# Kernel tuning notes

Measured on AMD Instinct MI355X. Metric: run time of the kernel, lower is better.

## Reference

```python
import jax, jax.numpy as jnp
import numpy as np

HEADS = 8
D_MODEL = 512

def setup_inputs() -> dict:
    key = jax.random.key(0)
    ks = jax.random.split(key, 7)
    t, w, h, b = 8, 14, 14, 8
    seq = t * w * h + 1  # 1569, includes CLS token
    q = jax.random.normal(ks[0], (seq, b, D_MODEL), jnp.float32)
    k = jax.random.normal(ks[1], (seq, b, D_MODEL), jnp.float32)
    value = jax.random.normal(ks[2], (seq, b, D_MODEL), jnp.float32)
    in_proj_weight = jax.random.normal(ks[3], (3 * D_MODEL, D_MODEL), jnp.float32) * (D_MODEL ** -0.5)
    in_proj_bias = jax.random.normal(ks[4], (3 * D_MODEL,), jnp.float32) * 0.02
    out_w = jax.random.normal(ks[5], (D_MODEL, D_MODEL), jnp.float32) * (D_MODEL ** -0.5)
    out_b = jax.random.normal(ks[6], (D_MODEL,), jnp.float32) * 0.02
    return {"q": q, "k": k, "value": value,
            "in_proj_weight": in_proj_weight, "in_proj_bias": in_proj_bias,
            "out_w": out_w, "out_b": out_b, "t": t, "w": w, "h": h}

def _sdpa(q, k, v):
    # scaled dot-product attention over batched 3D tensors [B, L, dh]
    temp = q.shape[-1] ** 0.5
    scores = jnp.einsum('bqd,bkd->bqk', q, k) / temp
    a = jax.nn.softmax(scores, axis=-1)  # softmax over dim=2 == last dim
    return jnp.einsum('bqk,bkd->bqd', a, v), a

def reference(q, k, value, in_proj_weight, in_proj_bias, out_w, out_b, t, w, h):
    seq, b, c = q.shape
    H, dh, wh = HEADS, c // HEADS, w * h
    q_cls = q[:1]          # [1, b, c] passed through untouched
    x = q[1:]              # [t*wh, b, c]
    qkv = x @ in_proj_weight.T + in_proj_bias  # fused QKV proj
    qq, kk, vv = qkv[..., :c], qkv[..., c:2 * c], qkv[..., 2 * c:]
    to5 = lambda z: z.reshape(t, wh, b, H, dh)
    # spatial stage: batch = (H, b, t), attend over wh
    q_s = to5(qq).transpose(3, 2, 0, 1, 4).reshape(H * b * t, wh, dh)
    k_s = to5(kk).transpose(3, 2, 0, 1, 4).reshape(H * b * t, wh, dh)
    v_s = to5(vv).transpose(3, 2, 0, 1, 4).reshape(H * b * t, wh, dh)
    out_s, attn = _sdpa(q_s, k_s, v_s)
    # temporal stage: batch = (H, b, wh), attend over t; V comes from spatial output
    v_t = out_s.reshape(H, b, t, wh, dh).transpose(0, 1, 3, 2, 4).reshape(H * b * wh, t, dh)
    q_t = to5(qq).transpose(3, 2, 1, 0, 4).reshape(H * b * wh, t, dh)
    k_t = to5(kk).transpose(3, 2, 1, 0, 4).reshape(H * b * wh, t, dh)
    out_t, _ = _sdpa(q_t, k_t, v_t)
    # back to [t*wh, b, c]
    out = out_t.reshape(H, b, wh, t, dh).transpose(3, 2, 1, 0, 4).reshape(t * wh, b, c)
    out = out @ out_w.T + out_b
    return jnp.concatenate([q_cls, out], axis=0), attn
```

## Files before the change

kernel.cpp:

```cpp
#include <hip/hip_runtime.h>
#include <cstdint>
#include <cstddef>

typedef __bf16 bf16;
typedef __bf16 bf16x8 __attribute__((ext_vector_type(8)));
typedef __bf16 bf16x4 __attribute__((ext_vector_type(4)));
typedef float  f32x4  __attribute__((ext_vector_type(4)));

#define MFMA16(a, b, c) __builtin_amdgcn_mfma_f32_16x16x32_bf16(a, b, c, 0, 0, 0)

__device__ __forceinline__ void gl2lds16(const bf16* g, bf16* l) {
  __builtin_amdgcn_global_load_lds(
      (const __attribute__((address_space(1))) void*)g,
      (__attribute__((address_space(3))) void*)l, 16, 0, 0);
}

__device__ __forceinline__ void cvt4(const float* __restrict__ s, bf16* __restrict__ d) {
  f32x4 v = *(const f32x4*)s;
  bf16x4 o;
  o[0] = (bf16)v[0]; o[1] = (bf16)v[1]; o[2] = (bf16)v[2]; o[3] = (bf16)v[3];
  *(bf16x4*)d = o;
}

__global__ __launch_bounds__(256) void prep_kernel(
    const float* __restrict__ q, const float* __restrict__ win,
    const float* __restrict__ wout, float* __restrict__ out0,
    bf16* __restrict__ xb, bf16* __restrict__ wqb, bf16* __restrict__ wob) {
  long u = (long)blockIdx.x * 256 + threadIdx.x;
  const long NX4 = 1605632, NWQ4 = 196608, NWO4 = 65536, NQC4 = 1024;
  if (u < NX4) { cvt4(q + 4096 + u * 4, xb + u * 4); return; }
  u -= NX4;
  if (u < NWQ4) { cvt4(win + u * 4, wqb + u * 4); return; }
  u -= NWQ4;
  if (u < NWO4) { cvt4(wout + u * 4, wob + u * 4); return; }
  u -= NWO4;
  if (u < NQC4) { *(f32x4*)(out0 + u * 4) = *(const f32x4*)(q + u * 4); }
}

template <bool OUTF32>
__global__ __launch_bounds__(256) void gemm_bt(
    const bf16* __restrict__ A, const bf16* __restrict__ Bm,
    const float* __restrict__ bias, bf16* __restrict__ Cb,
    float* __restrict__ Cf, int N, int K, long coff) {
  __shared__ bf16 As[128 * 32];
  __shared__ bf16 Bs[128 * 32];
  const int tid = threadIdx.x;
  const int wid = tid >> 6, lane = tid & 63;
  const int lr = lane & 15, lg = lane >> 4;

  const int nwg = gridDim.x * gridDim.y;
  const int orig = blockIdx.y * gridDim.x + blockIdx.x;
  const int cpx = nwg >> 3;
  const int swz = (orig & 7) * cpx + (orig >> 3);
  const int m0 = (swz / gridDim.x) * 128;
  const int n0 = (swz % gridDim.x) * 128;

  const int wr = wid >> 1, wc = wid & 1;
  const int srow = lane >> 2;
  const int scol = (lane & 3) * 8;

  f32x4 acc[4][4] = {};

  for (int kt = 0; kt < K; kt += 32) {
    __syncthreads();
#pragma unroll
    for (int j = 0; j < 2; ++j) {
      int r0 = wid * 32 + j * 16;
      gl2lds16(A + (size_t)(m0 + r0 + srow) * K + kt + scol, As + r0 * 32);
      gl2lds16(Bm + (size_t)(n0 + r0 + srow) * K + kt + scol, Bs + r0 * 32);
    }
    __syncthreads();

    bf16x8 af[4], bfr[4];
#pragma unroll
    for (int m = 0; m < 4; ++m)
      af[m] = *(const bf16x8*)(As + (wr * 64 + m * 16 + lr) * 32 + lg * 8);
#pragma unroll
    for (int n = 0; n < 4; ++n)
      bfr[n] = *(const bf16x8*)(Bs + (wc * 64 + n * 16 + lr) * 32 + lg * 8);
#pragma unroll
    for (int m = 0; m < 4; ++m)
#pragma unroll
      for (int n = 0; n < 4; ++n)
        acc[m][n] = MFMA16(af[m], bfr[n], acc[m][n]);
  }

#pragma unroll
  for (int m = 0; m < 4; ++m) {
    int row = m0 + wr * 64 + m * 16 + lg * 4;
#pragma unroll
    for (int n = 0; n < 4; ++n) {
      int col = n0 + wc * 64 + n * 16 + lr;
      float bv = bias[col];
#pragma unroll
      for (int i = 0; i < 4; ++i) {
        float v = acc[m][n][i] + bv;
        if (OUTF32) Cf[coff + (size_t)(row + i) * N + col] = v;
        else        Cb[(size_t)(row + i) * N + col] = (bf16)v;
      }
    }
  }
}

__global__ __launch_bounds__(512) void spatial_attn(
    const bf16* __restrict__ qkv, float* __restrict__ attn_out,
    bf16* __restrict__ outs) {
  __shared__ bf16 Kl[224][72];
  __shared__ bf16 Vt[64][232];
  __shared__ bf16 Pl[8][16][232];

  const int tid = threadIdx.x;
  const int wid = tid >> 6, lane = tid & 63;
  const int lr = lane & 15, lg = lane >> 4;
  const int batch = blockIdx.x;
  const int ti = batch & 7;
  const int bb = (batch >> 3) & 7;
  const int h = batch >> 6;

  {
    const int p = (tid >> 3);
    const int c = (tid & 7) * 8;
    bf16 zz = (bf16)0.f;
    for (int r0 = 0; r0 < 224; r0 += 64) {
      int pp = r0 + p;
      bf16x8 kv = {zz, zz, zz, zz, zz, zz, zz, zz};
      bf16x8 vv = {zz, zz, zz, zz, zz, zz, zz, zz};
      if (pp < 196) {
        size_t ro = ((size_t)(ti * 196 + pp) * 8 + bb) * 1536 + h * 64 + c;
        kv = *(const bf16x8*)(qkv + ro + 512);
        vv = *(const bf16x8*)(qkv + ro + 1024);
      }
      if (pp < 224) {
        *(bf16x8*)&Kl[pp][c] = kv;
#pragma unroll
        for (int j = 0; j < 8; ++j) Vt[c + j][pp] = vv[j];
      }
    }
  }
  __syncthreads();

  for (int qt = wid; qt < 13; qt += 8) {
    bf16x8 aq[2];
    {
      int row = qt * 16 + lr;
      if (row > 195) row = 195;
      size_t ro = ((size_t)(ti * 196 + row) * 8 + bb) * 1536 + h * 64;
#pragma unroll
      for (int kk = 0; kk < 2; ++kk)
        aq[kk] = *(const bf16x8*)(qkv + ro + kk * 32 + lg * 8);
    }

    f32x4 s[14] = {};
#pragma unroll
    for (int nn = 0; nn < 14; ++nn) {
      bf16x8 bk0 = *(const bf16x8*)&Kl[nn * 16 + lr][lg * 8];
      bf16x8 bk1 = *(const bf16x8*)&Kl[nn * 16 + lr][32 + lg * 8];
      s[nn] = MFMA16(aq[0], bk0, s[nn]);
      s[nn] = MFMA16(aq[1], bk1, s[nn]);
    }

#pragma unroll
    for (int nn = 0; nn < 14; ++nn) {
      bool pad = (nn * 16 + lr >= 196);
#pragma unroll
      for (int i = 0; i < 4; ++i)
        s[nn][i] = pad ? -1e30f : s[nn][i] * 0.125f;
    }

    float rinv[4];
#pragma unroll
    for (int i = 0; i < 4; ++i) {
      float v = -1e30f;
#pragma unroll
      for (int nn = 0; nn < 14; ++nn) v = fmaxf(v, s[nn][i]);
#pragma unroll
      for (int d = 1; d < 16; d <<= 1) v = fmaxf(v, __shfl_xor(v, d));
      float sum = 0.f;
#pragma unroll
      for (int nn = 0; nn < 14; ++nn) {
        float e = __expf(s[nn][i] - v);
        s[nn][i] = e;
        sum += e;
      }
#pragma unroll
      for (int d = 1; d < 16; d <<= 1) sum += __shfl_xor(sum, d);
      rinv[i] = 1.f / sum;
    }

#pragma unroll
    for (int nn = 0; nn < 14; ++nn) {
      int col = nn * 16 + lr;
#pragma unroll
      for (int i = 0; i < 4; ++i) {
        float pv = s[nn][i] * rinv[i];
        int rl = lg * 4 + i;
        int row = qt * 16 + rl;
        if (row < 196 && col < 196)
          attn_out[(size_t)batch * 38416 + (size_t)row * 196 + col] = pv;
        Pl[wid][rl][col] = (bf16)pv;
      }
    }

    f32x4 o[4] = {};
#pragma unroll
    for (int kb = 0; kb < 7; ++kb) {
      bf16x8 pa = *(const bf16x8*)&Pl[wid][lr][kb * 32 + lg * 8];
#pragma unroll
      for (int nd = 0; nd < 4; ++nd) {
        bf16x8 vb = *(const bf16x8*)&Vt[nd * 16 + lr][kb * 32 + lg * 8];
        o[nd] = MFMA16(pa, vb, o[nd]);
      }
    }

#pragma unroll
    for (int i = 0; i < 4; ++i) {
      int p = qt * 16 + lg * 4 + i;
      if (p < 196) {
#pragma unroll
        for (int nd = 0; nd < 4; ++nd) {
          int d = nd * 16 + lr;
          outs[(((size_t)((h * 8 + bb) * 196 + p)) * 8 + ti) * 64 + d] =
              (bf16)o[nd][i];
        }
      }
    }
  }
}

__global__ __launch_bounds__(256) void temporal_attn(
    const bf16* __restrict__ qkv, const bf16* __restrict__ outs,
    bf16* __restrict__ outt) {
  __shared__ bf16 Ql[4][8][72];
  __shared__ bf16 Kc[4][8][72];
  __shared__ bf16 Vl[4][8][64];
  __shared__ float Ps[4][8][8];

  const int tid = threadIdx.x, wid = tid >> 6, lane = tid & 63;
  const int batch = blockIdx.x * 4 + wid;
  const int p = batch % 196;
  const int hb = batch / 196;
  const int bb = hb & 7, h = hb >> 3;

  const int ri = lane >> 3;
  const int c8 = lane & 7;
  {
    size_t ro = ((size_t)(ri * 196 + p) * 8 + bb) * 1536 + h * 64 + c8 * 8;
    *(bf16x8*)&Ql[wid][ri][c8 * 8] = *(const bf16x8*)(qkv + ro);
    *(bf16x8*)&Kc[wid][ri][c8 * 8] = *(const bf16x8*)(qkv + ro + 512);
    *(bf16x8*)&Vl[wid][ri][c8 * 8] =
        *(const bf16x8*)(outs + ((size_t)batch * 8 + ri) * 64 + c8 * 8);
  }
  __syncthreads();

  float s = 0.f;
#pragma unroll
  for (int d = 0; d < 64; d += 8) {
    bf16x8 qv = *(const bf16x8*)&Ql[wid][ri][d];
    bf16x8 kv = *(const bf16x8*)&Kc[wid][c8][d];
#pragma unroll
    for (int e = 0; e < 8; ++e) s += (float)qv[e] * (float)kv[e];
  }
  s *= 0.125f;
  float mxv = s;
#pragma unroll
  for (int d2 = 1; d2 < 8; d2 <<= 1) mxv = fmaxf(mxv, __shfl_xor(mxv, d2));
  float e = __expf(s - mxv);
  float sum = e;
#pragma unroll
  for (int d2 = 1; d2 < 8; d2 <<= 1) sum += __shfl_xor(sum, d2);
  Ps[wid][ri][c8] = e / sum;
  __syncthreads();

  const int d = lane;
#pragma unroll
  for (int ii = 0; ii < 8; ++ii) {
    float o = 0.f;
#pragma unroll
    for (int j = 0; j < 8; ++j) o += Ps[wid][ii][j] * (float)Vl[wid][j][d];
    outt[((size_t)(ii * 196 + p) * 8 + bb) * 512 + h * 64 + d] = (bf16)o;
  }
}

extern "C" void kernel_launch(void* const* d_in, const int* in_sizes, int n_in,
                              void* d_out, int out_size, void* d_ws,
                              size_t ws_size, hipStream_t stream) {
  (void)in_sizes; (void)n_in; (void)out_size; (void)ws_size;
  const float* q    = (const float*)d_in[0];
  const float* win  = (const float*)d_in[3];
  const float* bin  = (const float*)d_in[4];
  const float* wout = (const float*)d_in[5];
  const float* bout = (const float*)d_in[6];
  float* out0 = (float*)d_out;
  float* attn = out0 + 6426624L;

  bf16* qkv  = (bf16*)d_ws;
  bf16* outs = qkv + 19267584L;
  bf16* outt = outs + 6422528L;
  bf16* wob  = outt + 6422528L;

  bf16* xb  = (bf16*)attn;
  bf16* wqb = xb + 6422528L;

  prep_kernel<<<7300, 256, 0, stream>>>(q, win, wout, out0, xb, wqb, wob);
  gemm_bt<false><<<dim3(12, 98), 256, 0, stream>>>(xb, wqb, bin, qkv, nullptr,
                                                   1536, 512, 0);
  spatial_attn<<<512, 512, 0, stream>>>(qkv, attn, outs);
  temporal_attn<<<3136, 256, 0, stream>>>(qkv, outs, outt);
  gemm_bt<true><<<dim3(4, 98), 256, 0, stream>>>(outt, wob, bout, nullptr,
                                                 out0, 512, 512, 4096);
}
```

Before: 106.4 us.

## Transpose QK MFMA to keep P rows in registers, drop LDS P buffer

New measurement: 226.0 us. +112.3%, slower.

```diff
diff --git a/kernel.cpp b/kernel.cpp
--- a/kernel.cpp
+++ b/kernel.cpp
@@ -102,12 +102,11 @@
   }
 }
 
-__global__ __launch_bounds__(512) void spatial_attn(
+__global__ __launch_bounds__(512, 4) void spatial_attn(
     const bf16* __restrict__ qkv, float* __restrict__ attn_out,
     bf16* __restrict__ outs) {
   __shared__ bf16 Kl[224][72];
   __shared__ bf16 Vt[64][232];
-  __shared__ bf16 Pl[8][16][232];
 
   const int tid = threadIdx.x;
   const int wid = tid >> 6, lane = tid & 63;
@@ -140,10 +139,10 @@
   __syncthreads();
 
   for (int qt = wid; qt < 13; qt += 8) {
+    const int q = qt * 16 + lr;
     bf16x8 aq[2];
     {
-      int row = qt * 16 + lr;
-      if (row > 195) row = 195;
+      int row = q > 195 ? 195 : q;
       size_t ro = ((size_t)(ti * 196 + row) * 8 + bb) * 1536 + h * 64;
 #pragma unroll
       for (int kk = 0; kk < 2; ++kk)
@@ -155,60 +154,76 @@
     for (int nn = 0; nn < 14; ++nn) {
       bf16x8 bk0 = *(const bf16x8*)&Kl[nn * 16 + lr][lg * 8];
       bf16x8 bk1 = *(const bf16x8*)&Kl[nn * 16 + lr][32 + lg * 8];
-      s[nn] = MFMA16(aq[0], bk0, s[nn]);
-      s[nn] = MFMA16(aq[1], bk1, s[nn]);
+      s[nn] = MFMA16(bk0, aq[0], s[nn]);
+      s[nn] = MFMA16(bk1, aq[1], s[nn]);
     }
 
 #pragma unroll
     for (int nn = 0; nn < 14; ++nn) {
-      bool pad = (nn * 16 + lr >= 196);
+      bool pad = (nn * 16 + lg * 4 >= 196);
 #pragma unroll
       for (int i = 0; i < 4; ++i)
         s[nn][i] = pad ? -1e30f : s[nn][i] * 0.125f;
     }
 
-    float rinv[4];
-#pragma unroll
-    for (int i = 0; i < 4; ++i) {
-      float v = -1e30f;
-#pragma unroll
-      for (int nn = 0; nn < 14; ++nn) v = fmaxf(v, s[nn][i]);
-#pragma unroll
-      for (int d = 1; d < 16; d <<= 1) v = fmaxf(v, __shfl_xor(v, d));
-      float sum = 0.f;
-#pragma unroll
-      for (int nn = 0; nn < 14; ++nn) {
+    float v = -1e30f;
+#pragma unroll
+    for (int nn = 0; nn < 14; ++nn)
+#pragma unroll
+      for (int i = 0; i < 4; ++i) v = fmaxf(v, s[nn][i]);
+    v = fmaxf(v, __shfl_xor(v, 16));
+    v = fmaxf(v, __shfl_xor(v, 32));
+    float sum = 0.f;
+#pragma unroll
+    for (int nn = 0; nn < 14; ++nn)
+#pragma unroll
+      for (int i = 0; i < 4; ++i) {
         float e = __expf(s[nn][i] - v);
         s[nn][i] = e;
         sum += e;
       }
-#pragma unroll
-      for (int d = 1; d < 16; d <<= 1) sum += __shfl_xor(sum, d);
-      rinv[i] = 1.f / sum;
-    }
-
+    sum += __shfl_xor(sum, 16);
+    sum += __shfl_xor(sum, 32);
+    float rinv = 1.f / sum;
+
+    uint32_t pkx[14], pky[14];
 #pragma unroll
     for (int nn = 0; nn < 14; ++nn) {
-      int col = nn * 16 + lr;
-#pragma unroll
-      for (int i = 0; i < 4; ++i) {
-        float pv = s[nn][i] * rinv[i];
-        int rl = lg * 4 + i;
-        int row = qt * 16 + rl;
-        if (row < 196 && col < 196)
-          attn_out[(size_t)batch * 38416 + (size_t)row * 196 + col] = pv;
-        Pl[wid][rl][col] = (bf16)pv;
-      }
-    }
-
+#pragma unroll
+      for (int i = 0; i < 4; ++i) s[nn][i] *= rinv;
+      int kbase = nn * 16 + lg * 4;
+      if (q < 196 && kbase < 196)
+        *(f32x4*)(attn_out + (size_t)batch * 38416 + (size_t)q * 196 + kbase) =
+            s[nn];
+      union { bf16x4 h; uint2 u; } pk;
+      pk.h[0] = (bf16)s[nn][0]; pk.h[1] = (bf16)s[nn][1];
+      pk.h[2] = (bf16)s[nn][2]; pk.h[3] = (bf16)s[nn][3];
+      pkx[nn] = pk.u.x; pky[nn] = pk.u.y;
+    }
+
+    const int low = lr + 32 * (lg & 1);
+    const int high = low + 16;
+    const bool hiN = (lg >> 1) != 0;
     f32x4 o[4] = {};
 #pragma unroll
     for (int kb = 0; kb < 7; ++kb) {
-      bf16x8 pa = *(const bf16x8*)&Pl[wid][lr][kb * 32 + lg * 8];
+      uint32_t a0x = __shfl((int)pkx[2 * kb], low);
+      uint32_t a0y = __shfl((int)pky[2 * kb], low);
+      uint32_t a1x = __shfl((int)pkx[2 * kb + 1], low);
+      uint32_t a1y = __shfl((int)pky[2 * kb + 1], low);
+      uint32_t b0x = __shfl((int)pkx[2 * kb], high);
+      uint32_t b0y = __shfl((int)pky[2 * kb], high);
+      uint32_t b1x = __shfl((int)pkx[2 * kb + 1], high);
+      uint32_t b1y = __shfl((int)pky[2 * kb + 1], high);
+      union { uint32_t u[4]; bf16x8 h; } pa;
+      pa.u[0] = hiN ? a1x : a0x;
+      pa.u[1] = hiN ? a1y : a0y;
+      pa.u[2] = hiN ? b1x : b0x;
+      pa.u[3] = hiN ? b1y : b0y;
 #pragma unroll
       for (int nd = 0; nd < 4; ++nd) {
         bf16x8 vb = *(const bf16x8*)&Vt[nd * 16 + lr][kb * 32 + lg * 8];
-        o[nd] = MFMA16(pa, vb, o[nd]);
+        o[nd] = MFMA16(pa.h, vb, o[nd]);
       }
     }
 
```
